# Kernel optimization log

Measured on AMD Instinct MI355X. Metric: run time of the kernel, lower is better.

Reference implementation:

```python
import jax, jax.numpy as jnp
import numpy as np

B, S, E = 2, 2048, 2048
A, H = 2048, 16  # attention_dim, n_heads
HD = A // H      # head_dim = 128
ROPE_THETA = 10000.0


def setup_inputs() -> dict:
    key = jax.random.key(0)
    k1, k2, k3 = jax.random.split(key, 3)
    x = jax.random.normal(k1, (B, S, E), dtype=jnp.float32)
    W_qkv = jax.random.normal(k2, (E, 3 * A), dtype=jnp.float32) * 0.02
    W_out = jax.random.normal(k3, (A, E), dtype=jnp.float32) * 0.02
    return {"x": x, "W_qkv": W_qkv, "W_out": W_out}


def _apply_rope(x):
    # x: (B, H, S, D); interleaved rotary pairs (rotary-embedding-torch default)
    b, h, s, d = x.shape
    inv_freq = 1.0 / (ROPE_THETA ** (jnp.arange(0, d, 2, dtype=jnp.float32) / d))
    freqs = jnp.arange(s, dtype=jnp.float32)[:, None] * inv_freq[None, :]  # (S, D/2)
    cos, sin = jnp.cos(freqs), jnp.sin(freqs)
    xr = x.reshape(b, h, s, d // 2, 2)
    x1, x2 = xr[..., 0], xr[..., 1]
    o1 = x1 * cos - x2 * sin
    o2 = x1 * sin + x2 * cos
    return jnp.stack([o1, o2], axis=-1).reshape(b, h, s, d)


def reference(x, W_qkv, W_out):
    b, s, _ = x.shape
    qkv = (x @ W_qkv).reshape(b, s, 3, H, HD)          # (B,S,3,H,hd)
    qkv = jnp.moveaxis(qkv, 3, 1)                      # movedim(-2,1) -> (B,H,S,3,hd)
    q, k, v = qkv[..., 0, :], qkv[..., 1, :], qkv[..., 2, :]
    q = _apply_rope(q)
    k = _apply_rope(k)
    scale = 1.0 / jnp.sqrt(jnp.asarray(HD, dtype=x.dtype))
    scores = jnp.einsum("bhqd,bhkd->bhqk", q, k) * scale
    attn = jax.nn.softmax(scores, axis=-1)
    out = jnp.einsum("bhqk,bhkd->bhqd", attn, v)       # (B,H,S,hd)
    out = out.transpose(0, 2, 1, 3).reshape(b, s, A)   # (B,S,A)
    return out @ W_out
```

## Files before the change

### kernel.cpp

```cpp
#include <hip/hip_runtime.h>
#include <math.h>

typedef float  f32x4  __attribute__((ext_vector_type(4)));
typedef short  s16x8 __attribute__((ext_vector_type(8)));
typedef short  s16x4 __attribute__((ext_vector_type(4)));
typedef unsigned short u16;
typedef unsigned int u32;

static __device__ __forceinline__ u16 f32_to_bf16_rne(float f) {
    u32 u = __builtin_bit_cast(u32, f);
    u32 r = u + 0x7fffu + ((u >> 16) & 1u);
    return (u16)(r >> 16);
}
static __device__ __forceinline__ u32 pack_bf16_rhu(float a, float b) {
    u32 ua = __builtin_bit_cast(u32, a);
    u32 ub = __builtin_bit_cast(u32, b);
    return ((ua + 0x8000u) >> 16) | ((ub + 0x8000u) & 0xffff0000u);
}
static __device__ __forceinline__ float bf16_to_f32(u16 h) {
    return __builtin_bit_cast(float, (u32)h << 16);
}

static __device__ __forceinline__ void gl2lds16(const void* g, void* l) {
    __builtin_amdgcn_global_load_lds(
        (const __attribute__((address_space(1))) u32*)g,
        (__attribute__((address_space(3))) u32*)l, 16, 0, 0);
}

__global__ __launch_bounds__(256) void k_cast(const float* __restrict__ in,
                                              u16* __restrict__ out) {
    int i = (blockIdx.x * 256 + threadIdx.x) * 8;
    float4 a = *reinterpret_cast<const float4*>(in + i);
    float4 b = *reinterpret_cast<const float4*>(in + i + 4);
    s16x8 o;
    o[0] = (short)f32_to_bf16_rne(a.x); o[1] = (short)f32_to_bf16_rne(a.y);
    o[2] = (short)f32_to_bf16_rne(a.z); o[3] = (short)f32_to_bf16_rne(a.w);
    o[4] = (short)f32_to_bf16_rne(b.x); o[5] = (short)f32_to_bf16_rne(b.y);
    o[6] = (short)f32_to_bf16_rne(b.z); o[7] = (short)f32_to_bf16_rne(b.w);
    *reinterpret_cast<s16x8*>(out + i) = o;
}

__global__ __launch_bounds__(256) void k_transpose_cast(const float* __restrict__ in,
                                                        u16* __restrict__ out,
                                                        int R, int C) {
    __shared__ float TT[64 * 130];
    const int t = threadIdx.x;
    const int ct = blockIdx.x, rt = blockIdx.y;
    const int tr = t >> 4;
    const int tc = t & 15;
    float4 v[8];
#pragma unroll
    for (int u = 0; u < 8; ++u) {
        int r = u * 16 + tr;
        v[u] = *reinterpret_cast<const float4*>(in + (size_t)(rt * 128 + r) * C + ct * 64 + tc * 4);
    }
#pragma unroll
    for (int u = 0; u < 8; ++u) {
        int r = u * 16 + tr;
        TT[(tc * 4 + 0) * 130 + r] = v[u].x;
        TT[(tc * 4 + 1) * 130 + r] = v[u].y;
        TT[(tc * 4 + 2) * 130 + r] = v[u].z;
        TT[(tc * 4 + 3) * 130 + r] = v[u].w;
    }
    __syncthreads();
#pragma unroll
    for (int u = 0; u < 4; ++u) {
        int oc = u * 16 + tr;
        int r0 = tc * 8;
        s16x8 o;
#pragma unroll
        for (int e = 0; e < 8; ++e)
            o[e] = (short)f32_to_bf16_rne(TT[oc * 130 + r0 + e]);
        *reinterpret_cast<s16x8*>(out + (size_t)(ct * 64 + oc) * R + rt * 128 + r0) = o;
    }
}

template<bool BF16OUT, bool ROPE>
__global__ __launch_bounds__(512, 2) void k_gemm384(const u16* __restrict__ Amat,
                                                    const u16* __restrict__ Bt,
                                                    void* __restrict__ Cout,
                                                    int M, int N, int K) {
    __shared__ __align__(16) u16 As[2][128 * 64];
    __shared__ __align__(16) u16 Bs[2][384 * 64];
    const int t = threadIdx.x;
    const int lane = t & 63, wave = t >> 6;
    const int m16 = lane & 15, qd = lane >> 4;
    const int wr = wave >> 2, wc = wave & 3;
    const int srow = lane >> 3;
    const int sch = (lane & 7) ^ srow;

    int bx, by;
    if (gridDim.x == 16 && gridDim.y == 32) {
        int orig = blockIdx.y * gridDim.x + blockIdx.x;
        int xcd = orig & 7, loc = orig >> 3;
        int cx = xcd & 3, cy = xcd >> 2;
        bx = cx * 4 + (loc & 3);
        by = cy * 16 + (loc >> 2);
    } else {
        bx = blockIdx.x; by = blockIdx.y;
    }
    const size_t m0 = (size_t)by * 128, n0 = (size_t)bx * 384;

    const u16* Ab = Amat + m0 * (size_t)K;
    const u16* Bb = Bt + n0 * (size_t)K;
    const int NT = K >> 6;

    auto stage128 = [&](const u16* gbase, u16* lbase, int k0) {
        int rb0 = wave * 8;
        gl2lds16(gbase + (size_t)(rb0 + srow) * K + k0 + sch * 8, lbase + rb0 * 64);
        int rb1 = rb0 + 64;
        gl2lds16(gbase + (size_t)(rb1 + srow) * K + k0 + sch * 8, lbase + rb1 * 64);
    };

    f32x4 acc[4][6] = {};
    s16x8 af[4][2], bq[6][2];

    stage128(Bb,                   &Bs[0][0],        0);
    stage128(Bb + 128 * (size_t)K, &Bs[0][128 * 64], 0);
    stage128(Bb + 256 * (size_t)K, &Bs[0][256 * 64], 0);
    stage128(Ab,                   &As[0][0],        0);
    if (NT > 1) {
        stage128(Bb,                   &Bs[1][0],        64);
        stage128(Bb + 128 * (size_t)K, &Bs[1][128 * 64], 64);
        asm volatile("s_waitcnt vmcnt(4)" ::: "memory");
    } else {
        asm volatile("s_waitcnt vmcnt(0)" ::: "memory");
    }
    __builtin_amdgcn_s_barrier();

    for (int kt = 0; kt < NT; ++kt) {
        const int p = kt & 1;

#pragma unroll
        for (int i = 0; i < 4; ++i) {
            int ra = wr * 64 + i * 16 + m16;
            af[i][0] = *reinterpret_cast<const s16x8*>(&As[p][ra * 64 + ((qd)     ^ (ra & 7)) * 8]);
        }
#pragma unroll
        for (int j = 0; j < 6; ++j) {
            int rb = wc * 96 + j * 16 + m16;
            bq[j][0] = *reinterpret_cast<const s16x8*>(&Bs[p][rb * 64 + ((qd)     ^ (rb & 7)) * 8]);
        }
        if (kt + 1 < NT) stage128(Bb + 256 * (size_t)K, &Bs[p ^ 1][256 * 64], (kt + 1) << 6);
#pragma unroll
        for (int i = 0; i < 4; ++i) {
            int ra = wr * 64 + i * 16 + m16;
            af[i][1] = *reinterpret_cast<const s16x8*>(&As[p][ra * 64 + ((4 + qd) ^ (ra & 7)) * 8]);
        }
#pragma unroll
        for (int j = 0; j < 6; ++j) {
            int rb = wc * 96 + j * 16 + m16;
            bq[j][1] = *reinterpret_cast<const s16x8*>(&Bs[p][rb * 64 + ((4 + qd) ^ (rb & 7)) * 8]);
        }
        if (kt + 1 < NT) stage128(Ab, &As[p ^ 1][0], (kt + 1) << 6);

        __builtin_amdgcn_s_setprio(1);
#pragma unroll
        for (int i = 0; i < 4; ++i)
#pragma unroll
            for (int j = 0; j < 6; ++j)
                acc[i][j] = __builtin_amdgcn_mfma_f32_16x16x32_bf16(af[i][0], bq[j][0], acc[i][j], 0, 0, 0);
        __builtin_amdgcn_s_setprio(0);

        asm volatile("s_waitcnt lgkmcnt(0)" ::: "memory");
        __builtin_amdgcn_s_barrier();

        if (kt + 2 < NT) {
            stage128(Bb,                   &Bs[p][0],        (kt + 2) << 6);
            stage128(Bb + 128 * (size_t)K, &Bs[p][128 * 64], (kt + 2) << 6);
        }
        __builtin_amdgcn_s_setprio(1);
#pragma unroll
        for (int i = 0; i < 4; ++i)
#pragma unroll
            for (int j = 0; j < 6; ++j)
                acc[i][j] = __builtin_amdgcn_mfma_f32_16x16x32_bf16(af[i][1], bq[j][1], acc[i][j], 0, 0, 0);
        __builtin_amdgcn_s_setprio(0);
        if (kt + 2 < NT) {
            asm volatile("s_waitcnt vmcnt(4)" ::: "memory");
        } else {
            asm volatile("s_waitcnt vmcnt(0)" ::: "memory");
        }
        __builtin_amdgcn_s_barrier();
    }

    if (ROPE) {
        float invf[6];
#pragma unroll
        for (int j = 0; j < 6; ++j) {
            int pi = ((int)(n0 + wc * 96 + j * 16 + m16) & 127) >> 1;
            invf[j] = __expf(-0.14391156831f * (float)pi);
        }
#pragma unroll
        for (int i = 0; i < 4; ++i)
#pragma unroll
            for (int j = 0; j < 6; ++j) {
                size_t colbase = n0 + wc * 96 + j * 16;
                if (colbase < 4096) {
#pragma unroll
                    for (int r = 0; r < 4; ++r) {
                        float v = acc[i][j][r];
                        float pv = __shfl_xor(v, 1);
                        size_t row = m0 + wr * 64 + i * 16 + qd * 4 + r;
                        float f = (float)(int)(row & 2047) * invf[j];
                        float sn, cs;
                        __sincosf(f, &sn, &cs);
                        float res = (m16 & 1) ? fmaf(pv, sn, v * cs) : fmaf(v, cs, -pv * sn);
                        ((u16*)Cout)[row * N + colbase + m16] = f32_to_bf16_rne(res);
                    }
                } else {
#pragma unroll
                    for (int r = 0; r < 4; ++r) {
                        size_t row = m0 + wr * 64 + i * 16 + qd * 4 + r;
                        ((u16*)Cout)[row * N + colbase + m16] = f32_to_bf16_rne(acc[i][j][r]);
                    }
                }
            }
    } else {
#pragma unroll
        for (int i = 0; i < 4; ++i)
#pragma unroll
            for (int j = 0; j < 6; ++j)
#pragma unroll
                for (int r = 0; r < 4; ++r) {
                    size_t row = m0 + wr * 64 + i * 16 + qd * 4 + r;
                    size_t col = n0 + wc * 96 + j * 16 + m16;
                    if (BF16OUT)
                        ((u16*)Cout)[row * N + col] = f32_to_bf16_rne(acc[i][j][r]);
                    else
                        ((float*)Cout)[row * N + col] = acc[i][j][r];
                }
    }
}

__global__ __launch_bounds__(512, 2) void k_gemmo(const u16* __restrict__ Amat,
                                                  const u16* __restrict__ Bt,
                                                  float* __restrict__ Cout,
                                                  int M, int N, int K) {
    __shared__ __align__(16) u16 As[2][128 * 64];
    __shared__ __align__(16) u16 Bs[2][256 * 64];
    const int t = threadIdx.x;
    const int lane = t & 63, wave = t >> 6;
    const int m16 = lane & 15, qd = lane >> 4;
    const int wr = wave >> 2, wc = wave & 3;
    const int srow = lane >> 3;
    const int sch = (lane & 7) ^ srow;

    int bx, by;
    if (gridDim.x == 8 && gridDim.y == 32) {
        int orig = blockIdx.y * gridDim.x + blockIdx.x;
        int xcd = orig & 7, loc = orig >> 3;
        int cx = xcd & 1, cy = xcd >> 1;
        bx = cx * 4 + (loc & 3);
        by = cy * 8 + (loc >> 2);
    } else {
        bx = blockIdx.x; by = blockIdx.y;
    }
    const size_t m0 = (size_t)by * 128, n0 = (size_t)bx * 256;

    const u16* Ab = Amat + m0 * (size_t)K;
    const u16* Bb = Bt + n0 * (size_t)K;
    const int NT = K >> 6;

    auto stage128 = [&](const u16* gbase, u16* lbase, int k0) {
        int rb0 = wave * 8;
        gl2lds16(gbase + (size_t)(rb0 + srow) * K + k0 + sch * 8, lbase + rb0 * 64);
        int rb1 = rb0 + 64;
        gl2lds16(gbase + (size_t)(rb1 + srow) * K + k0 + sch * 8, lbase + rb1 * 64);
    };

    f32x4 acc[4][4] = {};
    s16x8 af[4][2], bq[4][2];

    stage128(Ab,                   &As[0][0],        0);
    stage128(Bb,                   &Bs[0][0],        0);
    stage128(Bb + 128 * (size_t)K, &Bs[0][128 * 64], 0);
    if (NT > 1) {
        stage128(Ab,               &As[1][0],        64);
        stage128(Bb,               &Bs[1][0],        64);
        asm volatile("s_waitcnt vmcnt(4)" ::: "memory");
    } else {
        asm volatile("s_waitcnt vmcnt(0)" ::: "memory");
    }
    __builtin_amdgcn_s_barrier();

    for (int kt = 0; kt < NT; ++kt) {
        const int p = kt & 1;

#pragma unroll
        for (int i = 0; i < 4; ++i) {
            int ra = wr * 64 + i * 16 + m16;
            af[i][0] = *reinterpret_cast<const s16x8*>(&As[p][ra * 64 + ((qd)     ^ (ra & 7)) * 8]);
        }
#pragma unroll
        for (int j = 0; j < 4; ++j) {
            int rb = wc * 64 + j * 16 + m16;
            bq[j][0] = *reinterpret_cast<const s16x8*>(&Bs[p][rb * 64 + ((qd)     ^ (rb & 7)) * 8]);
        }
        if (kt + 1 < NT) stage128(Bb + 128 * (size_t)K, &Bs[p ^ 1][128 * 64], (kt + 1) << 6);
#pragma unroll
        for (int i = 0; i < 4; ++i) {
            int ra = wr * 64 + i * 16 + m16;
            af[i][1] = *reinterpret_cast<const s16x8*>(&As[p][ra * 64 + ((4 + qd) ^ (ra & 7)) * 8]);
        }
#pragma unroll
        for (int j = 0; j < 4; ++j) {
            int rb = wc * 64 + j * 16 + m16;
            bq[j][1] = *reinterpret_cast<const s16x8*>(&Bs[p][rb * 64 + ((4 + qd) ^ (rb & 7)) * 8]);
        }

        __builtin_amdgcn_s_setprio(1);
#pragma unroll
        for (int i = 0; i < 4; ++i)
#pragma unroll
            for (int j = 0; j < 4; ++j)
                acc[i][j] = __builtin_amdgcn_mfma_f32_16x16x32_bf16(af[i][0], bq[j][0], acc[i][j], 0, 0, 0);
        __builtin_amdgcn_s_setprio(0);

        asm volatile("s_waitcnt lgkmcnt(0)" ::: "memory");
        __builtin_amdgcn_s_barrier();

        if (kt + 2 < NT) {
            stage128(Ab, &As[p][0], (kt + 2) << 6);
            stage128(Bb, &Bs[p][0], (kt + 2) << 6);
        }
        __builtin_amdgcn_s_setprio(1);
#pragma unroll
        for (int i = 0; i < 4; ++i)
#pragma unroll
            for (int j = 0; j < 4; ++j)
                acc[i][j] = __builtin_amdgcn_mfma_f32_16x16x32_bf16(af[i][1], bq[j][1], acc[i][j], 0, 0, 0);
        __builtin_amdgcn_s_setprio(0);
        if (kt + 2 < NT) {
            asm volatile("s_waitcnt vmcnt(4)" ::: "memory");
        } else {
            asm volatile("s_waitcnt vmcnt(0)" ::: "memory");
        }
        __builtin_amdgcn_s_barrier();
    }

#pragma unroll
    for (int i = 0; i < 4; ++i)
#pragma unroll
        for (int j = 0; j < 4; ++j)
#pragma unroll
            for (int r = 0; r < 4; ++r) {
                size_t row = m0 + wr * 64 + i * 16 + qd * 4 + r;
                size_t col = n0 + wc * 64 + j * 16 + m16;
                Cout[row * N + col] = acc[i][j][r];
            }
}

__global__ __launch_bounds__(256) void k_transpose_v(const u16* __restrict__ qkv,
                                                     u16* __restrict__ vt) {
    __shared__ u16 TT[128 * 130];
    const int t = threadIdx.x;
    const int st = blockIdx.x;
    const int bh = blockIdx.y;
    const int b = bh >> 4, h = bh & 15;
    const u16* src = qkv + (size_t)b * 2048 * 6144 + 4096 + (size_t)h * 128;
    const int tr = t >> 4, tc = t & 15;
    s16x8 v[8];
#pragma unroll
    for (int u = 0; u < 8; ++u) {
        int s = u * 16 + tr;
        v[u] = *reinterpret_cast<const s16x8*>(src + (size_t)(st * 128 + s) * 6144 + tc * 8);
    }
#pragma unroll
    for (int u = 0; u < 8; ++u) {
        int s = u * 16 + tr;
#pragma unroll
        for (int e = 0; e < 8; ++e)
            TT[(tc * 8 + e) * 130 + s] = (u16)v[u][e];
    }
    __syncthreads();
    u16* dst = vt + (size_t)bh * 128 * 2048 + st * 128;
#pragma unroll
    for (int u = 0; u < 8; ++u) {
        int d = u * 16 + tr;
        int s0 = tc * 8;
        s16x8 o;
#pragma unroll
        for (int e = 0; e < 8; ++e) o[e] = (short)TT[d * 130 + s0 + e];
        *reinterpret_cast<s16x8*>(dst + (size_t)d * 2048 + s0) = o;
    }
}

__global__ __launch_bounds__(512, 4) void k_flash(const u16* __restrict__ qkv,
                                                  const u16* __restrict__ vt,
                                                  u16* __restrict__ out) {
    __shared__ __align__(16) u16 KS[128 * 136];
    __shared__ __align__(16) u16 VS[128 * 136];
    const int t = threadIdx.x, lane = t & 63, wave = t >> 6;
    const int m16 = lane & 15, qd = lane >> 4;
    const int bh = blockIdx.y, b = bh >> 4, h = bh & 15;
    const int q0 = blockIdx.x * 128;
    const u16* Qg = qkv + (size_t)b * 2048 * 6144 + (size_t)h * 128;
    const u16* Kg = Qg + 2048;
    const u16* Vtg = vt + (size_t)bh * 128 * 2048;
    const float C2 = 0.12751743f;

    int srow[4], scol[4], pi0[4];
#pragma unroll
    for (int ci = 0; ci < 4; ++ci) {
        int idx = ci * 512 + t;
        int row = idx >> 4, c = idx & 15;
        srow[ci] = row;
        scol[ci] = c * 8;
        pi0[ci] = 32 * (c >> 2) + 16 * (c & 1) + 4 * ((c >> 1) & 1);
    }

    s16x8 qf[4];
#pragma unroll
    for (int kc = 0; kc < 4; ++kc)
        qf[kc] = *reinterpret_cast<const s16x8*>(
            Qg + (size_t)(q0 + wave * 16 + m16) * 6144 + kc * 32 + qd * 8);

    f32x4 accO[8] = {};
    float mrow = -1e30f, lrow = 0.f;

    for (int kt = 0; kt < 16; ++kt) {
        const int s0 = kt * 128;
        s16x8 kreg[4], vreg[4];
#pragma unroll
        for (int ci = 0; ci < 4; ++ci) {
            kreg[ci] = *reinterpret_cast<const s16x8*>(
                Kg + (size_t)(s0 + srow[ci]) * 6144 + scol[ci]);
            vreg[ci] = *reinterpret_cast<const s16x8*>(
                Vtg + (size_t)srow[ci] * 2048 + s0 + scol[ci]);
        }
        __syncthreads();
#pragma unroll
        for (int ci = 0; ci < 4; ++ci) {
            *reinterpret_cast<s16x8*>(&KS[srow[ci] * 136 + scol[ci]]) = kreg[ci];
            s16x4 lo = __builtin_shufflevector(vreg[ci], vreg[ci], 0, 1, 2, 3);
            s16x4 hi = __builtin_shufflevector(vreg[ci], vreg[ci], 4, 5, 6, 7);
            *reinterpret_cast<s16x4*>(&VS[srow[ci] * 136 + pi0[ci]]) = lo;
            *reinterpret_cast<s16x4*>(&VS[srow[ci] * 136 + pi0[ci] + 8]) = hi;
        }
        __syncthreads();

        f32x4 accS[8] = {};
#pragma unroll
        for (int kc = 0; kc < 4; ++kc)
#pragma unroll
            for (int nj = 0; nj < 8; ++nj) {
                s16x8 kf = *reinterpret_cast<const s16x8*>(
                    &KS[(nj * 16 + m16) * 136 + (kc * 4 + qd) * 8]);
                accS[nj] = __builtin_amdgcn_mfma_f32_16x16x32_bf16(kf, qf[kc], accS[nj], 0, 0, 0);
            }

        float mx = accS[0][0];
#pragma unroll
        for (int nj = 0; nj < 8; ++nj)
#pragma unroll
            for (int r = 0; r < 4; ++r) mx = fmaxf(mx, accS[nj][r]);
        mx *= C2;
        mx = fmaxf(mx, __shfl_xor(mx, 16));
        mx = fmaxf(mx, __shfl_xor(mx, 32));
        float mn = fmaxf(mrow, mx);
        float alpha = __builtin_amdgcn_exp2f(mrow - mn);
        mrow = mn;
        float ls = 0.f;
        s16x4 pk[8];
#pragma unroll
        for (int nj = 0; nj < 8; ++nj) {
            float p0 = __builtin_amdgcn_exp2f(fmaf(accS[nj][0], C2, -mn));
            float p1 = __builtin_amdgcn_exp2f(fmaf(accS[nj][1], C2, -mn));
            float p2 = __builtin_amdgcn_exp2f(fmaf(accS[nj][2], C2, -mn));
            float p3 = __builtin_amdgcn_exp2f(fmaf(accS[nj][3], C2, -mn));
            ls += (p0 + p1) + (p2 + p3);
            u32 lo = pack_bf16_rhu(p0, p1);
            u32 hi = pack_bf16_rhu(p2, p3);
            uint2 pr = make_uint2(lo, hi);
            pk[nj] = __builtin_bit_cast(s16x4, pr);
        }
        ls += __shfl_xor(ls, 16);
        ls += __shfl_xor(ls, 32);
        lrow = lrow * alpha + ls;
        float aO[4];
#pragma unroll
        for (int r = 0; r < 4; ++r) aO[r] = __shfl(alpha, qd * 4 + r);
#pragma unroll
        for (int dj = 0; dj < 8; ++dj)
#pragma unroll
            for (int r = 0; r < 4; ++r) accO[dj][r] *= aO[r];

#pragma unroll
        for (int kb = 0; kb < 4; ++kb) {
            s16x8 af = __builtin_shufflevector(pk[2 * kb], pk[2 * kb + 1],
                                               0, 1, 2, 3, 4, 5, 6, 7);
#pragma unroll
            for (int dj = 0; dj < 8; ++dj) {
                s16x8 vf = *reinterpret_cast<const s16x8*>(
                    &VS[(dj * 16 + m16) * 136 + kb * 32 + qd * 8]);
                accO[dj] = __builtin_amdgcn_mfma_f32_16x16x32_bf16(af, vf, accO[dj], 0, 0, 0);
            }
        }
    }
    float invl = 1.0f / lrow;
    float iv[4];
#pragma unroll
    for (int r = 0; r < 4; ++r) iv[r] = __shfl(invl, qd * 4 + r);
#pragma unroll
    for (int r = 0; r < 4; ++r) {
        size_t row = (size_t)b * 2048 + q0 + wave * 16 + qd * 4 + r;
#pragma unroll
        for (int dj = 0; dj < 8; ++dj)
            out[row * 2048 + h * 128 + dj * 16 + m16] =
                f32_to_bf16_rne(accO[dj][r] * iv[r]);
    }
}

extern "C" void kernel_launch(void* const* d_in, const int* in_sizes, int n_in,
                              void* d_out, int out_size, void* d_ws, size_t ws_size,
                              hipStream_t stream) {
    const float* x     = (const float*)d_in[0];
    const float* W_qkv = (const float*)d_in[1];
    const float* W_out = (const float*)d_in[2];
    float* out = (float*)d_out;

    char* ws = (char*)d_ws;
    u16* xb   = (u16*)(ws);
    u16* Wqt  = (u16*)(ws + (16u << 20));
    u16* Wot  = (u16*)(ws + (40u << 20));
    u16* qkvb = (u16*)(ws + (48u << 20));
    u16* attn = (u16*)(ws + (96u << 20));
    u16* vtg  = (u16*)(ws + (112u << 20));

    k_cast<<<4096, 256, 0, stream>>>(x, xb);
    k_transpose_cast<<<dim3(96, 16), 256, 0, stream>>>(W_qkv, Wqt, 2048, 6144);
    k_transpose_cast<<<dim3(32, 16), 256, 0, stream>>>(W_out, Wot, 2048, 2048);
    k_gemm384<true, true><<<dim3(16, 32), 512, 0, stream>>>(xb, Wqt, qkvb, 4096, 6144, 2048);
    k_transpose_v<<<dim3(16, 32), 256, 0, stream>>>(qkvb, vtg);
    k_flash<<<dim3(16, 32), 512, 0, stream>>>(qkvb, vtg, attn);
    k_gemmo<<<dim3(8, 32), 512, 0, stream>>>(attn, Wot, out, 4096, 2048, 2048);
}
```

Before: 400.5 us.

## Merge prep kernels, fuse V transpose into QKV GEMM, prefetch K/V in flash

```diff
diff --git a/kernel.cpp b/kernel.cpp
--- a/kernel.cpp
+++ b/kernel.cpp
@@ -17,9 +17,6 @@
     u32 ub = __builtin_bit_cast(u32, b);
     return ((ua + 0x8000u) >> 16) | ((ub + 0x8000u) & 0xffff0000u);
 }
-static __device__ __forceinline__ float bf16_to_f32(u16 h) {
-    return __builtin_bit_cast(float, (u32)h << 16);
-}
 
 static __device__ __forceinline__ void gl2lds16(const void* g, void* l) {
     __builtin_amdgcn_global_load_lds(
@@ -27,27 +24,35 @@
         (__attribute__((address_space(3))) u32*)l, 16, 0, 0);
 }
 
-__global__ __launch_bounds__(256) void k_cast(const float* __restrict__ in,
-                                              u16* __restrict__ out) {
-    int i = (blockIdx.x * 256 + threadIdx.x) * 8;
-    float4 a = *reinterpret_cast<const float4*>(in + i);
-    float4 b = *reinterpret_cast<const float4*>(in + i + 4);
-    s16x8 o;
-    o[0] = (short)f32_to_bf16_rne(a.x); o[1] = (short)f32_to_bf16_rne(a.y);
-    o[2] = (short)f32_to_bf16_rne(a.z); o[3] = (short)f32_to_bf16_rne(a.w);
-    o[4] = (short)f32_to_bf16_rne(b.x); o[5] = (short)f32_to_bf16_rne(b.y);
-    o[6] = (short)f32_to_bf16_rne(b.z); o[7] = (short)f32_to_bf16_rne(b.w);
-    *reinterpret_cast<s16x8*>(out + i) = o;
-}
-
-__global__ __launch_bounds__(256) void k_transpose_cast(const float* __restrict__ in,
-                                                        u16* __restrict__ out,
-                                                        int R, int C) {
+__global__ __launch_bounds__(256) void k_prep(const float* __restrict__ x,
+                                              const float* __restrict__ Wq,
+                                              const float* __restrict__ Wo,
+                                              u16* __restrict__ xb,
+                                              u16* __restrict__ Wqt,
+                                              u16* __restrict__ Wot) {
     __shared__ float TT[64 * 130];
+    const int blk = blockIdx.x;
     const int t = threadIdx.x;
-    const int ct = blockIdx.x, rt = blockIdx.y;
-    const int tr = t >> 4;
-    const int tc = t & 15;
+    if (blk < 4096) {
+        int i = (blk * 256 + t) * 8;
+        float4 a = *reinterpret_cast<const float4*>(x + i);
+        float4 b = *reinterpret_cast<const float4*>(x + i + 4);
+        s16x8 o;
+        o[0] = (short)f32_to_bf16_rne(a.x); o[1] = (short)f32_to_bf16_rne(a.y);
+        o[2] = (short)f32_to_bf16_rne(a.z); o[3] = (short)f32_to_bf16_rne(a.w);
+        o[4] = (short)f32_to_bf16_rne(b.x); o[5] = (short)f32_to_bf16_rne(b.y);
+        o[6] = (short)f32_to_bf16_rne(b.z); o[7] = (short)f32_to_bf16_rne(b.w);
+        *reinterpret_cast<s16x8*>(xb + i) = o;
+        return;
+    }
+    const float* in; u16* out; int C, ct, rt;
+    if (blk < 5632) {
+        int tb = blk - 4096; ct = tb % 96; rt = tb / 96; in = Wq; out = Wqt; C = 6144;
+    } else {
+        int tb = blk - 5632; ct = tb % 32; rt = tb / 32; in = Wo; out = Wot; C = 2048;
+    }
+    const int R = 2048;
+    const int tr = t >> 4, tc = t & 15;
     float4 v[8];
 #pragma unroll
     for (int u = 0; u < 8; ++u) {
@@ -75,10 +80,10 @@
     }
 }
 
-template<bool BF16OUT, bool ROPE>
 __global__ __launch_bounds__(512, 2) void k_gemm384(const u16* __restrict__ Amat,
                                                     const u16* __restrict__ Bt,
-                                                    void* __restrict__ Cout,
+                                                    u16* __restrict__ Cout,
+                                                    u16* __restrict__ Vt,
                                                     int M, int N, int K) {
     __shared__ __align__(16) u16 As[2][128 * 64];
     __shared__ __align__(16) u16 Bs[2][384 * 64];
@@ -184,7 +189,7 @@
         __builtin_amdgcn_s_barrier();
     }
 
-    if (ROPE) {
+    {
         float invf[6];
 #pragma unroll
         for (int j = 0; j < 6; ++j) {
@@ -206,30 +211,22 @@
                         float sn, cs;
                         __sincosf(f, &sn, &cs);
                         float res = (m16 & 1) ? fmaf(pv, sn, v * cs) : fmaf(v, cs, -pv * sn);
-                        ((u16*)Cout)[row * N + colbase + m16] = f32_to_bf16_rne(res);
+                        Cout[row * N + colbase + m16] = f32_to_bf16_rne(res);
                     }
                 } else {
-#pragma unroll
-                    for (int r = 0; r < 4; ++r) {
-                        size_t row = m0 + wr * 64 + i * 16 + qd * 4 + r;
-                        ((u16*)Cout)[row * N + colbase + m16] = f32_to_bf16_rne(acc[i][j][r]);
-                    }
+                    int vcol = (int)colbase - 4096 + m16;
+                    int h = vcol >> 7, d = vcol & 127;
+                    size_t row0 = m0 + wr * 64 + i * 16 + qd * 4;
+                    int b = (int)(row0 >> 11);
+                    int s = (int)(row0 & 2047);
+                    s16x4 o;
+#pragma unroll
+                    for (int r = 0; r < 4; ++r)
+                        o[r] = (short)f32_to_bf16_rne(acc[i][j][r]);
+                    *reinterpret_cast<s16x4*>(
+                        Vt + ((size_t)(b * 16 + h)) * 262144 + (size_t)d * 2048 + s) = o;
                 }
             }
-    } else {
-#pragma unroll
-        for (int i = 0; i < 4; ++i)
-#pragma unroll
-            for (int j = 0; j < 6; ++j)
-#pragma unroll
-                for (int r = 0; r < 4; ++r) {
-                    size_t row = m0 + wr * 64 + i * 16 + qd * 4 + r;
-                    size_t col = n0 + wc * 96 + j * 16 + m16;
-                    if (BF16OUT)
-                        ((u16*)Cout)[row * N + col] = f32_to_bf16_rne(acc[i][j][r]);
-                    else
-                        ((float*)Cout)[row * N + col] = acc[i][j][r];
-                }
     }
 }
 
@@ -349,41 +346,6 @@
                 size_t col = n0 + wc * 64 + j * 16 + m16;
                 Cout[row * N + col] = acc[i][j][r];
             }
-}
-
-__global__ __launch_bounds__(256) void k_transpose_v(const u16* __restrict__ qkv,
-                                                     u16* __restrict__ vt) {
-    __shared__ u16 TT[128 * 130];
-    const int t = threadIdx.x;
-    const int st = blockIdx.x;
-    const int bh = blockIdx.y;
-    const int b = bh >> 4, h = bh & 15;
-    const u16* src = qkv + (size_t)b * 2048 * 6144 + 4096 + (size_t)h * 128;
-    const int tr = t >> 4, tc = t & 15;
-    s16x8 v[8];
-#pragma unroll
-    for (int u = 0; u < 8; ++u) {
-        int s = u * 16 + tr;
-        v[u] = *reinterpret_cast<const s16x8*>(src + (size_t)(st * 128 + s) * 6144 + tc * 8);
-    }
-#pragma unroll
-    for (int u = 0; u < 8; ++u) {
-        int s = u * 16 + tr;
-#pragma unroll
-        for (int e = 0; e < 8; ++e)
-            TT[(tc * 8 + e) * 130 + s] = (u16)v[u][e];
-    }
-    __syncthreads();
-    u16* dst = vt + (size_t)bh * 128 * 2048 + st * 128;
-#pragma unroll
-    for (int u = 0; u < 8; ++u) {
-        int d = u * 16 + tr;
-        int s0 = tc * 8;
-        s16x8 o;
-#pragma unroll
-        for (int e = 0; e < 8; ++e) o[e] = (short)TT[d * 130 + s0 + e];
-        *reinterpret_cast<s16x8*>(dst + (size_t)d * 2048 + s0) = o;
-    }
 }
 
 __global__ __launch_bounds__(512, 4) void k_flash(const u16* __restrict__ qkv,
@@ -419,16 +381,14 @@
     f32x4 accO[8] = {};
     float mrow = -1e30f, lrow = 0.f;
 
+    s16x8 kreg[4], vreg[4];
+#pragma unroll
+    for (int ci = 0; ci < 4; ++ci) {
+        kreg[ci] = *reinterpret_cast<const s16x8*>(Kg + (size_t)srow[ci] * 6144 + scol[ci]);
+        vreg[ci] = *reinterpret_cast<const s16x8*>(Vtg + (size_t)srow[ci] * 2048 + scol[ci]);
+    }
+
     for (int kt = 0; kt < 16; ++kt) {
-        const int s0 = kt * 128;
-        s16x8 kreg[4], vreg[4];
-#pragma unroll
-        for (int ci = 0; ci < 4; ++ci) {
-            kreg[ci] = *reinterpret_cast<const s16x8*>(
-                Kg + (size_t)(s0 + srow[ci]) * 6144 + scol[ci]);
-            vreg[ci] = *reinterpret_cast<const s16x8*>(
-                Vtg + (size_t)srow[ci] * 2048 + s0 + scol[ci]);
-        }
         __syncthreads();
 #pragma unroll
         for (int ci = 0; ci < 4; ++ci) {
@@ -441,6 +401,7 @@
         __syncthreads();
 
         f32x4 accS[8] = {};
+        __builtin_amdgcn_s_setprio(1);
 #pragma unroll
         for (int kc = 0; kc < 4; ++kc)
 #pragma unroll
@@ -449,6 +410,7 @@
                     &KS[(nj * 16 + m16) * 136 + (kc * 4 + qd) * 8]);
                 accS[nj] = __builtin_amdgcn_mfma_f32_16x16x32_bf16(kf, qf[kc], accS[nj], 0, 0, 0);
             }
+        __builtin_amdgcn_s_setprio(0);
 
         float mx = accS[0][0];
 #pragma unroll
@@ -475,6 +437,18 @@
             uint2 pr = make_uint2(lo, hi);
             pk[nj] = __builtin_bit_cast(s16x4, pr);
         }
+
+        if (kt + 1 < 16) {
+            const int sn = (kt + 1) * 128;
+#pragma unroll
+            for (int ci = 0; ci < 4; ++ci) {
+                kreg[ci] = *reinterpret_cast<const s16x8*>(
+                    Kg + (size_t)(sn + srow[ci]) * 6144 + scol[ci]);
+                vreg[ci] = *reinterpret_cast<const s16x8*>(
+                    Vtg + (size_t)srow[ci] * 2048 + sn + scol[ci]);
+            }
+        }
+
         ls += __shfl_xor(ls, 16);
         ls += __shfl_xor(ls, 32);
         lrow = lrow * alpha + ls;
@@ -486,6 +460,7 @@
 #pragma unroll
             for (int r = 0; r < 4; ++r) accO[dj][r] *= aO[r];
 
+        __builtin_amdgcn_s_setprio(1);
 #pragma unroll
         for (int kb = 0; kb < 4; ++kb) {
             s16x8 af = __builtin_shufflevector(pk[2 * kb], pk[2 * kb + 1],
@@ -497,6 +472,7 @@
                 accO[dj] = __builtin_amdgcn_mfma_f32_16x16x32_bf16(af, vf, accO[dj], 0, 0, 0);
             }
         }
+        __builtin_amdgcn_s_setprio(0);
     }
     float invl = 1.0f / lrow;
     float iv[4];
@@ -528,11 +504,8 @@
     u16* attn = (u16*)(ws + (96u << 20));
     u16* vtg  = (u16*)(ws + (112u << 20));
 
-    k_cast<<<4096, 256, 0, stream>>>(x, xb);
-    k_transpose_cast<<<dim3(96, 16), 256, 0, stream>>>(W_qkv, Wqt, 2048, 6144);
-    k_transpose_cast<<<dim3(32, 16), 256, 0, stream>>>(W_out, Wot, 2048, 2048);
-    k_gemm384<true, true><<<dim3(16, 32), 512, 0, stream>>>(xb, Wqt, qkvb, 4096, 6144, 2048);
-    k_transpose_v<<<dim3(16, 32), 256, 0, stream>>>(qkvb, vtg);
+    k_prep<<<6144, 256, 0, stream>>>(x, W_qkv, W_out, xb, Wqt, Wot);
+    k_gemm384<<<dim3(16, 32), 512, 0, stream>>>(xb, Wqt, qkvb, vtg, 4096, 6144, 2048);
     k_flash<<<dim3(16, 32), 512, 0, stream>>>(qkvb, vtg, attn);
     k_gemmo<<<dim3(8, 32), 512, 0, stream>>>(attn, Wot, out, 4096, 2048, 2048);
 }
```

Result: slower. 472.7 us (+18.0%).
